# Kernel optimization log

Measured on AMD Instinct MI355X. Metric: run time of the kernel, lower is better.

Reference implementation:

```python
import jax, jax.numpy as jnp
import numpy as np

N_HEADS = 2
HEAD_DIM = 32
SCALE = HEAD_DIM ** -0.5


def group_linear(x, w):
    # x: (S, B, din), w: (n_blocks, din_b, dout_b) block-diagonal linear
    S, B, _ = x.shape
    nb, din_b, dout_b = w.shape
    xb = x.reshape(S, B, nb, din_b)
    yb = jnp.einsum('sbnd,nde->sbne', xb, w)
    return yb.reshape(S, B, nb * dout_b)


def setup_inputs() -> dict:
    key = jax.random.key(0)
    ks = jax.random.split(key, 5)
    S, B, dim, nb = 2048, 16, 1024, 8
    block_din = dim // nb          # 128
    emb_b = HEAD_DIM * N_HEADS     # 64 per block
    x = jax.random.normal(ks[0], (S, B, dim), dtype=jnp.float32)
    wq = 0.01 * jax.random.normal(ks[1], (nb, block_din, emb_b), dtype=jnp.float32)
    wk = 0.01 * jax.random.normal(ks[2], (nb, block_din, emb_b), dtype=jnp.float32)
    wv = 0.01 * jax.random.normal(ks[3], (nb, block_din, emb_b), dtype=jnp.float32)
    wf = 0.01 * jax.random.normal(ks[4], (nb, emb_b, block_din), dtype=jnp.float32)
    return {'x': x, 'wq': wq, 'wk': wk, 'wv': wv, 'wf': wf}


def reference(x, wq, wk, wv, wf):
    S, B, dim = x.shape
    nb = wq.shape[0]
    # block-diagonal QKV projections -> (S, B, nb, n_heads, head_dim)
    q = group_linear(x, wq).reshape(S, B, nb, N_HEADS, HEAD_DIM)
    k = group_linear(x, wk).reshape(S, B, nb, N_HEADS, HEAD_DIM)
    v = group_linear(x, wv).reshape(S, B, nb, N_HEADS, HEAD_DIM)
    # attention over the n_blocks axis; heads leading: (S, B, h, nb, hd)
    q = jnp.swapaxes(q, 2, 3) * SCALE
    k = jnp.swapaxes(k, 2, 3)
    v = jnp.swapaxes(v, 2, 3)
    score = jnp.einsum('sbhnd,sbhmd->sbhnm', q, k)  # (S,B,h,nb,nb)
    score = jax.nn.softmax(score, axis=-1)
    out = jnp.einsum('sbhnm,sbhmd->sbhnd', score, v)
    out = jnp.swapaxes(out, 2, 3).reshape(S, B, nb * N_HEADS * HEAD_DIM)
    out = group_linear(out, wf)
    return out.reshape(S, B, dim)
```

## Files before the change

### kernel.cpp

```cpp
#include <hip/hip_runtime.h>
#include <math.h>

using short8  = __attribute__((ext_vector_type(8))) short;
using ushort8 = __attribute__((ext_vector_type(8))) unsigned short;
using f32x4   = __attribute__((ext_vector_type(4))) float;

constexpr int DIM = 1024, NB = 8, NH = 2, HD = 32;
constexpr float SCALE = 0.17677669529663687f;
constexpr int SXW = 1032;
constexpr int SQW = 1544;

__device__ __forceinline__ unsigned short f2bf(float f) {
  unsigned u = __float_as_uint(f);
  u += 0x7fff + ((u >> 16) & 1);
  return (unsigned short)(u >> 16);
}
__device__ __forceinline__ float bf2f(unsigned short h) {
  return __uint_as_float((unsigned)h << 16);
}
__device__ __forceinline__ unsigned pack2bf(float lo, float hi) {
  return (unsigned)f2bf(lo) | ((unsigned)f2bf(hi) << 16);
}

__global__ __launch_bounds__(256) void prep_weights(
    const float* __restrict__ wq, const float* __restrict__ wk,
    const float* __restrict__ wv, const float* __restrict__ wf,
    unsigned short* __restrict__ ws)
{
  int gid = blockIdx.x * 256 + threadIdx.x;
  if (gid < 196608) {
    int t = gid >> 11, r = gid & 2047;
    int s = r >> 9, l = (r >> 3) & 63, z = r & 7;
    int met = t >> 3, n = t & 7, m = met >> 2, et = met & 3;
    int fr = l & 15, fg = l >> 4;
    int e = et * 16 + fr, k = s * 32 + fg * 8 + z;
    const float* w = (m == 0) ? wq : (m == 1) ? wk : wv;
    float v = w[n * 8192 + k * 64 + e];
    if (m == 0) v *= SCALE;
    ws[gid] = f2bf(v);
  } else {
    int g2 = gid - 196608;
    int t = g2 >> 10, r = g2 & 1023;
    int s = r >> 9, l = (r >> 3) & 63, z = r & 7;
    int n = t >> 3, et = t & 7;
    int fr = l & 15, fg = l >> 4;
    int eo = et * 16 + fr, k = s * 32 + fg * 8 + z;
    ws[gid] = f2bf(wf[n * 8192 + k * 128 + eo]);
  }
}

__global__ __launch_bounds__(512, 6) void gc_fused(
    const float* __restrict__ x,
    const unsigned short* __restrict__ wsw,
    const unsigned short* __restrict__ wsf,
    float* __restrict__ out)
{
  __shared__ __align__(16) unsigned short smem[16 * SQW];

  const int tid  = threadIdx.x;
  const int lane = tid & 63;
  const int w    = tid >> 6;
  const int fr   = lane & 15;
  const int fg   = lane >> 4;
  const long tok0 = (long)blockIdx.x * 16;

  {
    const float* xb = x + tok0 * DIM;
    float4 xa[4], xc[4];
    #pragma unroll
    for (int jj = 0; jj < 4; ++jj) {
      int chunk = tid + 512 * jj;
      const float* src = xb + (long)(chunk >> 7) * DIM + (chunk & 127) * 8;
      xa[jj] = *reinterpret_cast<const float4*>(src);
      xc[jj] = *reinterpret_cast<const float4*>(src + 4);
    }
    #pragma unroll
    for (int jj = 0; jj < 4; ++jj) {
      int chunk = tid + 512 * jj;
      ushort8 v;
      v[0] = f2bf(xa[jj].x); v[1] = f2bf(xa[jj].y);
      v[2] = f2bf(xa[jj].z); v[3] = f2bf(xa[jj].w);
      v[4] = f2bf(xc[jj].x); v[5] = f2bf(xc[jj].y);
      v[6] = f2bf(xc[jj].z); v[7] = f2bf(xc[jj].w);
      *reinterpret_cast<ushort8*>(&smem[(chunk >> 7) * SXW + (chunk & 127) * 8]) = v;
    }
  }
  __syncthreads();

  ushort4 qreg[12];
  {
    short8 wfr[2][4];
    const unsigned short* wp0 = wsw + (w * 12) * 2048 + lane * 8;
    #pragma unroll
    for (int s = 0; s < 4; ++s)
      wfr[0][s] = *reinterpret_cast<const short8*>(wp0 + s * 512);
    #pragma unroll
    for (int j = 0; j < 12; ++j) {
      const int cc = w * 12 + j;
      const int n  = cc & 7;
      if (j < 11) {
        const unsigned short* wpn = wsw + (cc + 1) * 2048 + lane * 8;
        #pragma unroll
        for (int s = 0; s < 4; ++s)
          wfr[(j + 1) & 1][s] = *reinterpret_cast<const short8*>(wpn + s * 512);
      }
      short8 bfr[4];
      #pragma unroll
      for (int s = 0; s < 4; ++s)
        bfr[s] = *reinterpret_cast<const short8*>(&smem[fr * SXW + n * 128 + s * 32 + fg * 8]);
      f32x4 acc = {0.f, 0.f, 0.f, 0.f};
      #pragma unroll
      for (int s = 0; s < 4; ++s)
        acc = __builtin_amdgcn_mfma_f32_16x16x32_bf16(wfr[j & 1][s], bfr[s], acc, 0, 0, 0);
      ushort4 d4;
      d4.x = f2bf(acc[0]); d4.y = f2bf(acc[1]);
      d4.z = f2bf(acc[2]); d4.w = f2bf(acc[3]);
      qreg[j] = d4;
    }
  }
  __syncthreads();

  {
    #pragma unroll
    for (int j = 0; j < 12; ++j) {
      const int cc = w * 12 + j;
      const int met = cc >> 3, n = cc & 7;
      const int m = met >> 2, e0 = (met & 3) * 16;
      if (m < 2) {
        *reinterpret_cast<ushort4*>(&smem[fr * SQW + m * 512 + n * 64 + e0 + fg * 4]) = qreg[j];
      } else {
        const unsigned short vals[4] = {qreg[j].x, qreg[j].y, qreg[j].z, qreg[j].w};
        #pragma unroll
        for (int r = 0; r < 4; ++r) {
          int e = e0 + fg * 4 + r, dd = e & 31, h = e >> 5;
          smem[fr * SQW + 1024 + dd * 16 + h * 8 + n] = vals[r];
        }
      }
    }
  }
  __syncthreads();

  {
    const int la = lane & 15, ga = lane >> 4;
    const int rowoff = (la & 7) * 64 + (la >> 3) * 32;
    const bool useful = ((ga >> 1) == (la >> 3));
    const bool kvalid = (ga < 2);
    const int srcA = (ga * 32 + la) & 63;
    #pragma unroll
    for (int tt = 0; tt < 2; ++tt) {
      const int t = w * 2 + tt;
      const unsigned short* tb = &smem[t * SQW];
      short8 kfr = *reinterpret_cast<const short8*>(tb + 512 + rowoff + ga * 8);
      short8 qfr = *reinterpret_cast<const short8*>(tb + rowoff + ga * 8);
      f32x4 zero = {0.f, 0.f, 0.f, 0.f};
      f32x4 s = __builtin_amdgcn_mfma_f32_16x16x32_bf16(kfr, qfr, zero, 0, 0, 0);
      float m4 = fmaxf(fmaxf(s[0], s[1]), fmaxf(s[2], s[3]));
      float mx = fmaxf(m4, __shfl_xor(m4, 16));
      float e0 = __expf(s[0] - mx), e1 = __expf(s[1] - mx);
      float e2 = __expf(s[2] - mx), e3 = __expf(s[3] - mx);
      float sm  = e0 + e1 + e2 + e3;
      float smt = sm + __shfl_xor(sm, 16);
      float inv = useful ? (1.f / smt) : 0.f;
      unsigned pk01 = pack2bf(e0 * inv, e1 * inv);
      unsigned pk23 = pack2bf(e2 * inv, e3 * inv);
      unsigned b0 = (unsigned)__builtin_amdgcn_ds_bpermute(srcA * 4, (int)pk01);
      unsigned b1 = (unsigned)__builtin_amdgcn_ds_bpermute(srcA * 4, (int)pk23);
      unsigned b2 = (unsigned)__builtin_amdgcn_ds_bpermute(((srcA + 16) & 63) * 4, (int)pk01);
      unsigned b3 = (unsigned)__builtin_amdgcn_ds_bpermute(((srcA + 16) & 63) * 4, (int)pk23);
      union { unsigned u[4]; short8 s8; } pb;
      pb.u[0] = kvalid ? b0 : 0u;  pb.u[1] = kvalid ? b1 : 0u;
      pb.u[2] = kvalid ? b2 : 0u;  pb.u[3] = kvalid ? b3 : 0u;
      #pragma unroll
      for (int dh = 0; dh < 2; ++dh) {
        short8 va = *reinterpret_cast<const short8*>(
            tb + 1024 + (dh * 16 + la) * 16 + (ga & 1) * 8);
        f32x4 o = __builtin_amdgcn_mfma_f32_16x16x32_bf16(va, pb.s8, zero, 0, 0, 0);
        ushort4 ou;
        ou.x = f2bf(o[0]); ou.y = f2bf(o[1]); ou.z = f2bf(o[2]); ou.w = f2bf(o[3]);
        *reinterpret_cast<ushort4*>(
            &smem[t * SQW + (la & 7) * 64 + (la >> 3) * 32 + dh * 16 + ga * 4]) = ou;
      }
    }
  }
  __syncthreads();

  {
    const int n = w;
    short8 bfr[2];
    #pragma unroll
    for (int s = 0; s < 2; ++s)
      bfr[s] = *reinterpret_cast<const short8*>(&smem[fr * SQW + n * 64 + s * 32 + fg * 8]);
    #pragma unroll
    for (int et = 0; et < 8; ++et) {
      const unsigned short* wp = wsf + (n * 8 + et) * 1024 + lane * 8;
      f32x4 acc = {0.f, 0.f, 0.f, 0.f};
      #pragma unroll
      for (int s = 0; s < 2; ++s) {
        short8 af = *reinterpret_cast<const short8*>(wp + s * 512);
        acc = __builtin_amdgcn_mfma_f32_16x16x32_bf16(af, bfr[s], acc, 0, 0, 0);
      }
      float4 o; o.x = acc[0]; o.y = acc[1]; o.z = acc[2]; o.w = acc[3];
      *reinterpret_cast<float4*>(out + (tok0 + fr) * DIM + n * 128 + et * 16 + fg * 4) = o;
    }
  }
}

extern "C" void kernel_launch(void* const* d_in, const int* in_sizes, int n_in,
                              void* d_out, int out_size, void* d_ws, size_t ws_size,
                              hipStream_t stream) {
  const float* x  = (const float*)d_in[0];
  const float* wq = (const float*)d_in[1];
  const float* wk = (const float*)d_in[2];
  const float* wv = (const float*)d_in[3];
  const float* wf = (const float*)d_in[4];
  float* out = (float*)d_out;
  unsigned short* ws = (unsigned short*)d_ws;

  prep_weights<<<dim3(1024), dim3(256), 0, stream>>>(wq, wk, wv, wf, ws);

  const int tokens = in_sizes[0] / DIM;
  gc_fused<<<dim3(tokens / 16), dim3(512), 0, stream>>>(x, ws, ws + 196608, out);
}
```

Measured before the change: 86.89 us.

## Swizzle Q/K/V shared layout, deepen weight prefetch, hoist output-projection weight loads

Introduces an XOR-swizzled shared-memory layout for Q/K (and the attention output) plus a new V layout split by head, to reduce LDS bank conflicts in the scatter and fragment reads. The QKV projection now keeps four weight fragments in flight instead of double-buffering, and the final projection loads all eight weight tiles before its MFMA loop. Launch bounds drop from 6 to 4 waves-per-SIMD hint to give room for the extra registers, trading occupancy for more memory-level parallelism.

New measurement: 90.39 us. +4.0%, slower.

```diff
diff --git a/kernel.cpp b/kernel.cpp
--- a/kernel.cpp
+++ b/kernel.cpp
@@ -20,6 +20,10 @@
 }
 __device__ __forceinline__ unsigned pack2bf(float lo, float hi) {
   return (unsigned)f2bf(lo) | ((unsigned)f2bf(hi) << 16);
+}
+
+__device__ __forceinline__ int qk_off(int R, int blk, int sub) {
+  return R * 32 + ((blk ^ (R & 3)) * 8) + sub;
 }
 
 __global__ __launch_bounds__(256) void prep_weights(
@@ -49,7 +53,7 @@
   }
 }
 
-__global__ __launch_bounds__(512, 6) void gc_fused(
+__global__ __launch_bounds__(512, 4) void gc_fused(
     const float* __restrict__ x,
     const unsigned short* __restrict__ wsw,
     const unsigned short* __restrict__ wsf,
@@ -89,21 +93,17 @@
 
   ushort4 qreg[12];
   {
-    short8 wfr[2][4];
-    const unsigned short* wp0 = wsw + (w * 12) * 2048 + lane * 8;
-    #pragma unroll
-    for (int s = 0; s < 4; ++s)
-      wfr[0][s] = *reinterpret_cast<const short8*>(wp0 + s * 512);
+    short8 wfrag[4][4];
+    #pragma unroll
+    for (int p = 0; p < 4; ++p) {
+      const unsigned short* wp = wsw + (w * 12 + p) * 2048 + lane * 8;
+      #pragma unroll
+      for (int s = 0; s < 4; ++s)
+        wfrag[p][s] = *reinterpret_cast<const short8*>(wp + s * 512);
+    }
     #pragma unroll
     for (int j = 0; j < 12; ++j) {
-      const int cc = w * 12 + j;
-      const int n  = cc & 7;
-      if (j < 11) {
-        const unsigned short* wpn = wsw + (cc + 1) * 2048 + lane * 8;
-        #pragma unroll
-        for (int s = 0; s < 4; ++s)
-          wfr[(j + 1) & 1][s] = *reinterpret_cast<const short8*>(wpn + s * 512);
-      }
+      const int n = (w * 12 + j) & 7;
       short8 bfr[4];
       #pragma unroll
       for (int s = 0; s < 4; ++s)
@@ -111,7 +111,13 @@
       f32x4 acc = {0.f, 0.f, 0.f, 0.f};
       #pragma unroll
       for (int s = 0; s < 4; ++s)
-        acc = __builtin_amdgcn_mfma_f32_16x16x32_bf16(wfr[j & 1][s], bfr[s], acc, 0, 0, 0);
+        acc = __builtin_amdgcn_mfma_f32_16x16x32_bf16(wfrag[j & 3][s], bfr[s], acc, 0, 0, 0);
+      if (j + 4 < 12) {
+        const unsigned short* wp = wsw + (w * 12 + j + 4) * 2048 + lane * 8;
+        #pragma unroll
+        for (int s = 0; s < 4; ++s)
+          wfrag[j & 3][s] = *reinterpret_cast<const short8*>(wp + s * 512);
+      }
       ushort4 d4;
       d4.x = f2bf(acc[0]); d4.y = f2bf(acc[1]);
       d4.z = f2bf(acc[2]); d4.w = f2bf(acc[3]);
@@ -127,13 +133,17 @@
       const int met = cc >> 3, n = cc & 7;
       const int m = met >> 2, e0 = (met & 3) * 16;
       if (m < 2) {
-        *reinterpret_cast<ushort4*>(&smem[fr * SQW + m * 512 + n * 64 + e0 + fg * 4]) = qreg[j];
+        const int e00 = e0 + fg * 4;
+        const int h = e00 >> 5, dd0 = e00 & 31;
+        const int R = 2 * n + h;
+        *reinterpret_cast<ushort4*>(
+            &smem[fr * SQW + m * 512 + qk_off(R, dd0 >> 3, dd0 & 7)]) = qreg[j];
       } else {
         const unsigned short vals[4] = {qreg[j].x, qreg[j].y, qreg[j].z, qreg[j].w};
         #pragma unroll
         for (int r = 0; r < 4; ++r) {
-          int e = e0 + fg * 4 + r, dd = e & 31, h = e >> 5;
-          smem[fr * SQW + 1024 + dd * 16 + h * 8 + n] = vals[r];
+          const int e = e0 + fg * 4 + r, dd = e & 31, h = e >> 5;
+          smem[fr * SQW + 1024 + h * 256 + dd * 8 + n] = vals[r];
         }
       }
     }
@@ -142,7 +152,8 @@
 
   {
     const int la = lane & 15, ga = lane >> 4;
-    const int rowoff = (la & 7) * 64 + (la >> 3) * 32;
+    const int R  = 2 * (la & 7) + (la >> 3);
+    const int qoff = qk_off(R, ga, 0);
     const bool useful = ((ga >> 1) == (la >> 3));
     const bool kvalid = (ga < 2);
     const int srcA = (ga * 32 + la) & 63;
@@ -150,8 +161,8 @@
     for (int tt = 0; tt < 2; ++tt) {
       const int t = w * 2 + tt;
       const unsigned short* tb = &smem[t * SQW];
-      short8 kfr = *reinterpret_cast<const short8*>(tb + 512 + rowoff + ga * 8);
-      short8 qfr = *reinterpret_cast<const short8*>(tb + rowoff + ga * 8);
+      short8 kfr = *reinterpret_cast<const short8*>(tb + 512 + qoff);
+      short8 qfr = *reinterpret_cast<const short8*>(tb + qoff);
       f32x4 zero = {0.f, 0.f, 0.f, 0.f};
       f32x4 s = __builtin_amdgcn_mfma_f32_16x16x32_bf16(kfr, qfr, zero, 0, 0, 0);
       float m4 = fmaxf(fmaxf(s[0], s[1]), fmaxf(s[2], s[3]));
@@ -173,12 +184,13 @@
       #pragma unroll
       for (int dh = 0; dh < 2; ++dh) {
         short8 va = *reinterpret_cast<const short8*>(
-            tb + 1024 + (dh * 16 + la) * 16 + (ga & 1) * 8);
+            tb + 1024 + (ga & 1) * 256 + (dh * 16 + la) * 8);
         f32x4 o = __builtin_amdgcn_mfma_f32_16x16x32_bf16(va, pb.s8, zero, 0, 0, 0);
         ushort4 ou;
         ou.x = f2bf(o[0]); ou.y = f2bf(o[1]); ou.z = f2bf(o[2]); ou.w = f2bf(o[3]);
+        const int blk = 2 * dh + (ga >> 1);
         *reinterpret_cast<ushort4*>(
-            &smem[t * SQW + (la & 7) * 64 + (la >> 3) * 32 + dh * 16 + ga * 4]) = ou;
+            &smem[t * SQW + qk_off(R, blk, (ga & 1) * 4)]) = ou;
       }
     }
   }
@@ -186,19 +198,25 @@
 
   {
     const int n = w;
-    short8 bfr[2];
-    #pragma unroll
-    for (int s = 0; s < 2; ++s)
-      bfr[s] = *reinterpret_cast<const short8*>(&smem[fr * SQW + n * 64 + s * 32 + fg * 8]);
+    short8 wfd[8][2];
     #pragma unroll
     for (int et = 0; et < 8; ++et) {
       const unsigned short* wp = wsf + (n * 8 + et) * 1024 + lane * 8;
+      wfd[et][0] = *reinterpret_cast<const short8*>(wp);
+      wfd[et][1] = *reinterpret_cast<const short8*>(wp + 512);
+    }
+    short8 bfr[2];
+    #pragma unroll
+    for (int s = 0; s < 2; ++s) {
+      const int R = 2 * n + s;
+      bfr[s] = *reinterpret_cast<const short8*>(&smem[fr * SQW + qk_off(R, fg, 0)]);
+    }
+    #pragma unroll
+    for (int et = 0; et < 8; ++et) {
       f32x4 acc = {0.f, 0.f, 0.f, 0.f};
       #pragma unroll
-      for (int s = 0; s < 2; ++s) {
-        short8 af = *reinterpret_cast<const short8*>(wp + s * 512);
-        acc = __builtin_amdgcn_mfma_f32_16x16x32_bf16(af, bfr[s], acc, 0, 0, 0);
-      }
+      for (int s = 0; s < 2; ++s)
+        acc = __builtin_amdgcn_mfma_f32_16x16x32_bf16(wfd[et][s], bfr[s], acc, 0, 0, 0);
       float4 o; o.x = acc[0]; o.y = acc[1]; o.z = acc[2]; o.w = acc[3];
       *reinterpret_cast<float4*>(out + (tok0 + fr) * DIM + n * 128 + et * 16 + fg * 4) = o;
     }
```
